# Kernel optimization log

Hardware: AMD Instinct MI355X
Metric: run time of the kernel (lower is better)

The kernel has to match this reference:

```python
import jax, jax.numpy as jnp
import numpy as np


def setup_inputs() -> dict:
    key = jax.random.key(0)
    k1, k2, k3 = jax.random.split(key, 3)
    B, C, S, Fin, Fout = 16, 64, 2048, 64, 64
    x = jax.random.normal(k1, (B, C, S, Fin), dtype=jnp.float32)
    # positive entries so row sums are > 0 and sqrt is well-defined
    adj = jax.random.uniform(k2, (C, C), dtype=jnp.float32)
    weight = jax.random.normal(k3, (Fin, Fout), dtype=jnp.float32) * (1.0 / np.sqrt(Fin))
    return {"x": x, "adj": adj, "weight": weight}


def reference(x, adj, weight):
    # Symmetric normalization: D^{-1/2} A D^{-1/2}. The torch code builds a
    # full diag + matrix inverse; mathematically this is elementwise rsqrt
    # row/col scaling of adj.
    d_inv_sqrt = jax.lax.rsqrt(jnp.sum(adj, axis=1))          # [C]
    norm_adj = adj * d_inv_sqrt[:, None] * d_inv_sqrt[None, :]  # [C, C]
    # support[b,c,s,o] = sum_f x[b,c,s,f] * weight[f,o]
    support = jnp.einsum('bcsf,fo->bcso', x, weight)
    # mix over channel (graph node) dim: out[b,c,s,o] = sum_d A_norm[c,d] support[b,d,s,o]
    out = jnp.einsum('cd,bdso->bcso', norm_adj, support)
    return jax.nn.relu(out)
```

## Files before the change

kernel.cpp:

```cpp
#include <hip/hip_runtime.h>
#include <hip/hip_bf16.h>

#define B_ 16
#define C_ 64
#define S_ 2048
#define F_ 64
#define SF (S_ * F_)

typedef __attribute__((ext_vector_type(8))) short short8;
typedef __attribute__((ext_vector_type(4))) float float4_;

#define SWZ(row, col) ((col) ^ (((row) & 7) << 3))
#define SWZ4(row, col) ((col) ^ (((row) & 7) << 2))

__device__ __forceinline__ unsigned short f2bf(float f) {
    unsigned int u = __builtin_bit_cast(unsigned int, f);
    u += 0x7fffu + ((u >> 16) & 1u);
    return (unsigned short)(u >> 16);
}

__global__ void gcn_prep(const float* __restrict__ adj, const float* __restrict__ wgt,
                         unsigned short* __restrict__ nadj, unsigned short* __restrict__ wT)
{
    __shared__ float dis[C_];
    const int t = threadIdx.x;
    if (t < C_) {
        float s = 0.f;
        for (int d = 0; d < C_; ++d) s += adj[t * C_ + d];
        dis[t] = rsqrtf(s);
    }
    __syncthreads();
    for (int i = t; i < C_ * C_; i += 256) {
        const int c = i >> 6, d = i & 63;
        nadj[i] = f2bf(adj[i] * dis[c] * dis[d]);
        wT[d * F_ + c] = f2bf(wgt[i]);
    }
}

__global__ __launch_bounds__(512, 4) void gcn_main(
    const float* __restrict__ x,
    const unsigned short* __restrict__ nadj,
    const unsigned short* __restrict__ wT,
    float* __restrict__ out)
{
    __shared__ __align__(16) unsigned short lds_nadj[C_ * C_];
    __shared__ __align__(16) unsigned short lds_wT[F_ * F_];
    __shared__ __align__(16) float obuf_all[8][16 * 64];

    const int tid  = threadIdx.x;
    const int w    = tid >> 6;
    const int l    = tid & 63;
    const int lrow = l & 15;
    const int lgrp = l >> 4;

    {
        const int fc = tid >> 3;
        const int fd = (tid & 7) * 8;
        *(short8*)(lds_nadj + fc * 64 + SWZ(fc, fd)) = *(const short8*)(nadj + fc * 64 + fd);
        *(short8*)(lds_wT  + fc * 64 + SWZ(fc, fd)) = *(const short8*)(wT  + fc * 64 + fd);
    }
    __syncthreads();

    const int b  = blockIdx.x >> 8;
    const int st = blockIdx.x & 255;
    const int s  = st * 8 + w;

    const float* xb = x + (size_t)b * C_ * SF + (size_t)s * F_;
    short8 af[4][2];
#pragma unroll
    for (int dt = 0; dt < 4; ++dt) {
        const float* xr = xb + (size_t)(dt * 16 + lrow) * SF;
#pragma unroll
        for (int ks = 0; ks < 2; ++ks) {
            float4_ u0 = __builtin_nontemporal_load((const float4_*)(xr + ks * 32 + lgrp * 8));
            float4_ u1 = __builtin_nontemporal_load((const float4_*)(xr + ks * 32 + lgrp * 8 + 4));
            short8 a;
#pragma unroll
            for (int j = 0; j < 4; ++j) {
                a[j]     = (short)f2bf(u0[j]);
                a[4 + j] = (short)f2bf(u1[j]);
            }
            af[dt][ks] = a;
        }
    }

    float* myO = obuf_all[w];
    unsigned short* myT = (unsigned short*)myO;

    short8 aA[4][2];
#pragma unroll
    for (int ot = 0; ot < 4; ++ot) {
        const int orow = ot * 16 + lrow;
        short8 wf0 = *(const short8*)(lds_wT + orow * 64 + SWZ(lrow, lgrp * 8));
        short8 wf1 = *(const short8*)(lds_wT + orow * 64 + SWZ(lrow, 32 + lgrp * 8));
#pragma unroll
        for (int dt = 0; dt < 4; ++dt) {
            float4_ s1 = {0.f, 0.f, 0.f, 0.f};
            s1 = __builtin_amdgcn_mfma_f32_16x16x32_bf16(af[dt][0], wf0, s1, 0, 0, 0);
            s1 = __builtin_amdgcn_mfma_f32_16x16x32_bf16(af[dt][1], wf1, s1, 0, 0, 0);
            const int dbase = dt * 16 + lgrp * 4;
            uint2 pk;
            pk.x = (unsigned)f2bf(s1[0]) | ((unsigned)f2bf(s1[1]) << 16);
            pk.y = (unsigned)f2bf(s1[2]) | ((unsigned)f2bf(s1[3]) << 16);
            *(uint2*)(myT + lrow * 64 + SWZ(lrow, dbase)) = pk;
        }
        aA[ot][0] = *(const short8*)(myT + lrow * 64 + SWZ(lrow, lgrp * 8));
        aA[ot][1] = *(const short8*)(myT + lrow * 64 + SWZ(lrow, 32 + lgrp * 8));
    }

#pragma unroll 1
    for (int ct = 0; ct < 4; ++ct) {
        const int crow = ct * 16 + lrow;
        short8 an0 = *(const short8*)(lds_nadj + crow * 64 + SWZ(lrow, lgrp * 8));
        short8 an1 = *(const short8*)(lds_nadj + crow * 64 + SWZ(lrow, 32 + lgrp * 8));

#pragma unroll
        for (int ot = 0; ot < 4; ++ot) {
            float4_ acc = {0.f, 0.f, 0.f, 0.f};
            acc = __builtin_amdgcn_mfma_f32_16x16x32_bf16(aA[ot][0], an0, acc, 0, 0, 0);
            acc = __builtin_amdgcn_mfma_f32_16x16x32_bf16(aA[ot][1], an1, acc, 0, 0, 0);
            float4_ r;
#pragma unroll
            for (int j = 0; j < 4; ++j) r[j] = fmaxf(acc[j], 0.f);
            *(float4_*)(myO + lrow * 64 + SWZ4(lrow, ot * 16 + lgrp * 4)) = r;
        }

#pragma unroll
        for (int t = 0; t < 4; ++t) {
            const int cl  = t * 4 + (l >> 4);
            const int col = (l & 15) * 4;
            float4_ v = *(const float4_*)(myO + cl * 64 + SWZ4(cl, col));
            float* g = out + ((size_t)(b * C_ + ct * 16 + cl) * S_ + s) * F_ + col;
            __builtin_nontemporal_store(v, (float4_*)g);
        }
    }
}

extern "C" void kernel_launch(void* const* d_in, const int* in_sizes, int n_in,
                              void* d_out, int out_size, void* d_ws, size_t ws_size,
                              hipStream_t stream) {
    const float* x   = (const float*)d_in[0];
    const float* adj = (const float*)d_in[1];
    const float* wgt = (const float*)d_in[2];
    float* out = (float*)d_out;

    unsigned short* nadj = (unsigned short*)d_ws;
    unsigned short* wT   = nadj + C_ * C_;

    gcn_prep<<<1, 256, 0, stream>>>(adj, wgt, nadj, wT);

    dim3 grid(B_ * (S_ / 8));
    gcn_main<<<grid, 512, 0, stream>>>(x, nadj, wT, out);
}
```

Before: 226.5 us.

## Stage block outputs as bf16 in shared LDS for contiguous per-channel stores

```diff
diff --git a/kernel.cpp b/kernel.cpp
--- a/kernel.cpp
+++ b/kernel.cpp
@@ -11,7 +11,6 @@
 typedef __attribute__((ext_vector_type(4))) float float4_;
 
 #define SWZ(row, col) ((col) ^ (((row) & 7) << 3))
-#define SWZ4(row, col) ((col) ^ (((row) & 7) << 2))
 
 __device__ __forceinline__ unsigned short f2bf(float f) {
     unsigned int u = __builtin_bit_cast(unsigned int, f);
@@ -45,7 +44,7 @@
 {
     __shared__ __align__(16) unsigned short lds_nadj[C_ * C_];
     __shared__ __align__(16) unsigned short lds_wT[F_ * F_];
-    __shared__ __align__(16) float obuf_all[8][16 * 64];
+    __shared__ __align__(16) unsigned short obuf[C_ * 8 * 64];
 
     const int tid  = threadIdx.x;
     const int w    = tid >> 6;
@@ -84,8 +83,7 @@
         }
     }
 
-    float* myO = obuf_all[w];
-    unsigned short* myT = (unsigned short*)myO;
+    unsigned short* myT = obuf + w * 1024;
 
     short8 aA[4][2];
 #pragma unroll
@@ -107,31 +105,42 @@
         aA[ot][0] = *(const short8*)(myT + lrow * 64 + SWZ(lrow, lgrp * 8));
         aA[ot][1] = *(const short8*)(myT + lrow * 64 + SWZ(lrow, 32 + lgrp * 8));
     }
+    __syncthreads();
 
 #pragma unroll 1
     for (int ct = 0; ct < 4; ++ct) {
         const int crow = ct * 16 + lrow;
         short8 an0 = *(const short8*)(lds_nadj + crow * 64 + SWZ(lrow, lgrp * 8));
         short8 an1 = *(const short8*)(lds_nadj + crow * 64 + SWZ(lrow, 32 + lgrp * 8));
-
 #pragma unroll
         for (int ot = 0; ot < 4; ++ot) {
             float4_ acc = {0.f, 0.f, 0.f, 0.f};
             acc = __builtin_amdgcn_mfma_f32_16x16x32_bf16(aA[ot][0], an0, acc, 0, 0, 0);
             acc = __builtin_amdgcn_mfma_f32_16x16x32_bf16(aA[ot][1], an1, acc, 0, 0, 0);
-            float4_ r;
-#pragma unroll
-            for (int j = 0; j < 4; ++j) r[j] = fmaxf(acc[j], 0.f);
-            *(float4_*)(myO + lrow * 64 + SWZ4(lrow, ot * 16 + lgrp * 4)) = r;
+            const int o = ot * 16 + lgrp * 4;
+            uint2 pk;
+            pk.x = (unsigned)f2bf(fmaxf(acc[0], 0.f)) | ((unsigned)f2bf(fmaxf(acc[1], 0.f)) << 16);
+            pk.y = (unsigned)f2bf(fmaxf(acc[2], 0.f)) | ((unsigned)f2bf(fmaxf(acc[3], 0.f)) << 16);
+            *(uint2*)(obuf + crow * 512 + w * 64 + (o ^ ((crow & 7) << 3))) = pk;
         }
+    }
+    __syncthreads();
 
 #pragma unroll
-        for (int t = 0; t < 4; ++t) {
-            const int cl  = t * 4 + (l >> 4);
-            const int col = (l & 15) * 4;
-            float4_ v = *(const float4_*)(myO + cl * 64 + SWZ4(cl, col));
-            float* g = out + ((size_t)(b * C_ + ct * 16 + cl) * S_ + s) * F_ + col;
-            __builtin_nontemporal_store(v, (float4_*)g);
+    for (int cr = 0; cr < 8; ++cr) {
+        const int c = w * 8 + cr;
+        float* grow = out + ((size_t)(b * C_ + c) * S_ + st * 8) * F_;
+#pragma unroll
+        for (int ph = 0; ph < 2; ++ph) {
+            const int sl = ph * 4 + (l >> 4);
+            const int o  = (l & 15) * 4;
+            uint2 v = *(const uint2*)(obuf + c * 512 + sl * 64 + (o ^ ((c & 7) << 3)));
+            float4_ r;
+            r[0] = __builtin_bit_cast(float, v.x << 16);
+            r[1] = __builtin_bit_cast(float, v.x & 0xFFFF0000u);
+            r[2] = __builtin_bit_cast(float, v.y << 16);
+            r[3] = __builtin_bit_cast(float, v.y & 0xFFFF0000u);
+            __builtin_nontemporal_store(r, (float4_*)(grow + ph * 256 + l * 4));
         }
     }
 }
```

Result: slower. 235.7 us (+4.1%).
